# Performance work log

Hardware: AMD Instinct MI355X
Metric: run time of the kernel (lower is better)

Reference implementation:

```python
import jax, jax.numpy as jnp
import numpy as np

N_TABLES = 26
VOCAB = 100000
M_SPA = 64
B = 8192
N_DENSE = 13
N_FEAT = N_TABLES + 1  # 27 features entering interaction
LI, LJ = np.tril_indices(N_FEAT, k=-1)  # strictly-lower pairs, matches torch li/lj order


def setup_inputs() -> dict:
    key = jax.random.key(0)
    ks = jax.random.split(key, 16)
    dense_x = jax.random.normal(ks[0], (B, N_DENSE), dtype=jnp.float32)
    lS_i = jax.random.randint(ks[1], (N_TABLES, B), 0, VOCAB, dtype=jnp.int64)
    # one index per bag -> offsets are arange(B) for every table
    lS_o = jnp.tile(jnp.arange(B, dtype=jnp.int64)[None, :], (N_TABLES, 1))
    # embedding tables, uniform(-sqrt(1/n), sqrt(1/n)) as in create_emb
    s = np.sqrt(1.0 / VOCAB)
    Wemb = jax.random.uniform(ks[2], (N_TABLES, VOCAB, M_SPA), dtype=jnp.float32, minval=-s, maxval=s)

    def mk_lin(k, n, m):
        k1, k2 = jax.random.split(k)
        W = jax.random.normal(k1, (m, n), dtype=jnp.float32) * np.sqrt(2.0 / (m + n))
        b = jax.random.normal(k2, (m,), dtype=jnp.float32) * np.sqrt(1.0 / m)
        return W, b

    bW0, bb0 = mk_lin(ks[3], 13, 512)
    bW1, bb1 = mk_lin(ks[4], 512, 256)
    bW2, bb2 = mk_lin(ks[5], 256, 64)
    tW0, tb0 = mk_lin(ks[6], 415, 512)
    tW1, tb1 = mk_lin(ks[7], 512, 256)
    tW2, tb2 = mk_lin(ks[8], 256, 1)
    return dict(dense_x=dense_x, lS_i=lS_i, lS_o=lS_o, Wemb=Wemb,
                bW0=bW0, bb0=bb0, bW1=bW1, bb1=bb1, bW2=bW2, bb2=bb2,
                tW0=tW0, tb0=tb0, tW1=tW1, tb1=tb1, tW2=tW2, tb2=tb2)


def reference(dense_x, lS_i, lS_o, Wemb,
              bW0, bb0, bW1, bb1, bW2, bb2,
              tW0, tb0, tW1, tb1, tW2, tb2):
    # bottom MLP (all ReLU, sigmoid_bot=-1)
    x = jax.nn.relu(dense_x @ bW0.T + bb0)
    x = jax.nn.relu(x @ bW1.T + bb1)
    x = jax.nn.relu(x @ bW2.T + bb2)  # [B, 64]
    # multi-table EmbeddingBag(sum) with one index per bag == plain gather
    ly = jax.vmap(lambda W, idx: W[idx])(Wemb, lS_i)  # [26, B, 64]
    # dot interaction
    T = jnp.concatenate([x[:, None, :], jnp.transpose(ly, (1, 0, 2))], axis=1)  # [B, 27, 64]
    Z = jnp.einsum('bnd,bmd->bnm', T, T)  # [B, 27, 27]
    Zflat = Z[:, LI, LJ]  # [B, 351]
    R = jnp.concatenate([x, Zflat], axis=1)  # [B, 415]
    # top MLP: ReLU, ReLU, Sigmoid (sigmoid_top=2)
    z = jax.nn.relu(R @ tW0.T + tb0)
    z = jax.nn.relu(z @ tW1.T + tb1)
    p = jax.nn.sigmoid(z @ tW2.T + tb2)  # [B, 1]
    # loss_threshold = 0.0 -> no clamp
    return p
```

## Files before the change

### kernel.cpp

```cpp
#include <hip/hip_runtime.h>
#include <hip/hip_bf16.h>


typedef _Float16 f16x8 __attribute__((ext_vector_type(8)));
typedef float f32x4 __attribute__((ext_vector_type(4)));

__device__ __forceinline__ f16x8 cvt8(float4 a, float4 b) {
  f16x8 f;
  f[0] = (_Float16)a.x; f[1] = (_Float16)a.y;
  f[2] = (_Float16)a.z; f[3] = (_Float16)a.w;
  f[4] = (_Float16)b.x; f[5] = (_Float16)b.y;
  f[6] = (_Float16)b.z; f[7] = (_Float16)b.w;
  return f;
}

__device__ __forceinline__ void tile_store_frag(
    _Float16* __restrict__ dst, const float* __restrict__ src,
    int i, int Ksrc, int NKK)
{
  int e = i & 7;
  int lane = (i >> 3) & 63;
  int rc = lane & 15, g = lane >> 4;
  int q = i >> 9;
  int kk = q % NKK;
  int j = q / NKK;
  int c = j * 16 + rc;
  int k = kk * 32 + g * 8 + e;
  dst[i] = (_Float16)((k < Ksrc) ? src[(size_t)c * Ksrc + k] : 0.0f);
}

__global__ __launch_bounds__(256) void prep_kernel(
    const float* __restrict__ bW0, const float* __restrict__ bW1,
    const float* __restrict__ bW2, const float* __restrict__ tW0,
    const float* __restrict__ tW1,
    _Float16* __restrict__ w0, _Float16* __restrict__ w1,
    _Float16* __restrict__ w2, _Float16* __restrict__ t0,
    _Float16* __restrict__ t1)
{
  int i = blockIdx.x * 256 + threadIdx.x;
  if (i < 16384)  { tile_store_frag(w0, bW0, i, 13, 1);   return; }
  i -= 16384;
  if (i < 131072) { tile_store_frag(w1, bW1, i, 512, 16); return; }
  i -= 131072;
  if (i < 16384)  { tile_store_frag(w2, bW2, i, 256, 8);  return; }
  i -= 16384;
  if (i < 229376) { tile_store_frag(t0, tW0, i, 415, 14); return; }
  i -= 229376;
  if (i < 131072) { tile_store_frag(t1, tW1, i, 512, 16); return; }
}

__global__ __launch_bounds__(512, 2) void fused_kernel(
    const float* __restrict__ dense, const int* __restrict__ lSi,
    const float* __restrict__ Wemb,
    const _Float16* __restrict__ w0, const float* __restrict__ bb0,
    const _Float16* __restrict__ w1, const float* __restrict__ bb1,
    const _Float16* __restrict__ w2, const float* __restrict__ bb2,
    const _Float16* __restrict__ t0w, const float* __restrict__ tb0,
    const _Float16* __restrict__ t1w, const float* __restrict__ tb1,
    const float* __restrict__ tW2, const float* __restrict__ tb2,
    float* __restrict__ out)
{
  __shared__ __align__(16) char regA[32768];
  __shared__ __align__(16) char regB[28672];
  _Float16* x1s = (_Float16*)regA;
  _Float16* x3s = (_Float16*)regA;
  _Float16* z1s = (_Float16*)regA;
  float*    dns = (float*)regB;
  _Float16* x2s = (_Float16*)regB;
  _Float16* Rs  = (_Float16*)regB;
  float*    psm = (float*)regB;

  const int t = threadIdx.x;
  const int lane = t & 63, wv = t >> 6;
  const int rc = lane & 15, g = lane >> 4;
  const int ko = g * 8;
  const int sw = (rc & 7) << 3;
  const int b0 = blockIdx.x * 32;

  if (t < 416) {
    int r = t / 13, c = t - r * 13;
    dns[r * 16 + c] = dense[(size_t)b0 * 13 + t];
  } else if (t < 512) {
    int q = t - 416;
    int r = q / 3, c = 13 + (q - r * 3);
    dns[r * 16 + c] = 0.0f;
  }
  __syncthreads();

  {
    f16x8 af[2];
#pragma unroll
    for (int rt = 0; rt < 2; ++rt) {
      f16x8 a = {};
      if (g < 2) {
        const float* s = &dns[(rt * 16 + rc) * 16 + ko];
        a = cvt8(*(const float4*)s, *(const float4*)(s + 4));
      }
      af[rt] = a;
    }
    f32x4 acc[2][4] = {};
#pragma unroll
    for (int j = 0; j < 4; ++j) {
      const int jb = wv * 4 + j;
      f16x8 wf = *(const f16x8*)&w0[(size_t)(jb * 64 + lane) * 8];
#pragma unroll
      for (int rt = 0; rt < 2; ++rt)
        acc[rt][j] = __builtin_amdgcn_mfma_f32_16x16x32_f16(af[rt], wf, acc[rt][j], 0, 0, 0);
    }
#pragma unroll
    for (int j = 0; j < 4; ++j) {
      const int col = wv * 64 + j * 16 + rc;
      const float bs = bb0[col];
#pragma unroll
      for (int rt = 0; rt < 2; ++rt)
#pragma unroll
        for (int r = 0; r < 4; ++r) {
          int row = rt * 16 + g * 4 + r;
          float v = fmaxf(acc[rt][j][r] + bs, 0.0f);
          x1s[row * 512 + (col ^ ((row & 7) << 3))] = (_Float16)v;
        }
    }
  }
  __syncthreads();

  {
    f32x4 acc[2][2] = {};
#pragma unroll
    for (int kk = 0; kk < 16; ++kk) {
      f16x8 af[2];
#pragma unroll
      for (int rt = 0; rt < 2; ++rt)
        af[rt] = *(const f16x8*)&x1s[(rt * 16 + rc) * 512 + ((kk * 32 + ko) ^ sw)];
#pragma unroll
      for (int j = 0; j < 2; ++j) {
        const int jb = wv * 2 + j;
        f16x8 wf = *(const f16x8*)&w1[(size_t)((jb * 16 + kk) * 64 + lane) * 8];
#pragma unroll
        for (int rt = 0; rt < 2; ++rt)
          acc[rt][j] = __builtin_amdgcn_mfma_f32_16x16x32_f16(af[rt], wf, acc[rt][j], 0, 0, 0);
      }
    }
#pragma unroll
    for (int j = 0; j < 2; ++j) {
      const int col = wv * 32 + j * 16 + rc;
      const float bs = bb1[col];
#pragma unroll
      for (int rt = 0; rt < 2; ++rt)
#pragma unroll
        for (int r = 0; r < 4; ++r) {
          int row = rt * 16 + g * 4 + r;
          float v = fmaxf(acc[rt][j][r] + bs, 0.0f);
          x2s[row * 256 + (col ^ ((row & 7) << 3))] = (_Float16)v;
        }
    }
  }
  __syncthreads();

  if (wv < 4) {
    f32x4 acc[2] = {};
#pragma unroll
    for (int kk = 0; kk < 8; ++kk) {
      f16x8 wf = *(const f16x8*)&w2[(size_t)((wv * 8 + kk) * 64 + lane) * 8];
#pragma unroll
      for (int rt = 0; rt < 2; ++rt) {
        f16x8 af = *(const f16x8*)&x2s[(rt * 16 + rc) * 256 + ((kk * 32 + ko) ^ sw)];
        acc[rt] = __builtin_amdgcn_mfma_f32_16x16x32_f16(af, wf, acc[rt], 0, 0, 0);
      }
    }
    const int col = wv * 16 + rc;
    const float bs = bb2[col];
#pragma unroll
    for (int rt = 0; rt < 2; ++rt)
#pragma unroll
      for (int r = 0; r < 4; ++r) {
        int row = rt * 16 + g * 4 + r;
        float v = fmaxf(acc[rt][r] + bs, 0.0f);
        x3s[row * 64 + col] = (_Float16)v;
      }
  }
  __syncthreads();

  {
    int e_idx[4][2];
#pragma unroll
    for (int i = 0; i < 4; ++i) {
      const int b = b0 + wv * 4 + i;
#pragma unroll
      for (int rt = 0; rt < 2; ++rt) {
        const int gr = rt * 16 + rc;
        e_idx[i][rt] = (gr >= 1 && gr <= 26) ? lSi[(size_t)(gr - 1) * 8192 + b] : 0;
      }
    }
#pragma unroll
    for (int i = 0; i < 4; ++i) {
      const int bl = wv * 4 + i;
      const int swr = (bl & 7) << 3;
      f16x8 frag[2][2];
#pragma unroll
      for (int rt = 0; rt < 2; ++rt) {
        const int gr = rt * 16 + rc;
        if (gr == 0) {
          frag[rt][0] = *(const f16x8*)&x3s[bl * 64 + ko];
          frag[rt][1] = *(const f16x8*)&x3s[bl * 64 + 32 + ko];
        } else if (gr <= 26) {
          const float* src = Wemb + ((size_t)(gr - 1) * 100000 + (size_t)e_idx[i][rt]) * 64;
#pragma unroll
          for (int kh = 0; kh < 2; ++kh) {
            const float* s = src + kh * 32 + ko;
            frag[rt][kh] = cvt8(*(const float4*)s, *(const float4*)(s + 4));
          }
        } else {
          f16x8 z = {};
          frag[rt][0] = z; frag[rt][1] = z;
        }
      }
      f32x4 z00 = {}, z10 = {}, z11 = {};
#pragma unroll
      for (int kh = 0; kh < 2; ++kh) {
        z00 = __builtin_amdgcn_mfma_f32_16x16x32_f16(frag[0][kh], frag[0][kh], z00, 0, 0, 0);
        z10 = __builtin_amdgcn_mfma_f32_16x16x32_f16(frag[1][kh], frag[0][kh], z10, 0, 0, 0);
        z11 = __builtin_amdgcn_mfma_f32_16x16x32_f16(frag[1][kh], frag[1][kh], z11, 0, 0, 0);
      }
      Rs[bl * 448 + (lane ^ swr)] = x3s[bl * 64 + lane];
      if (lane < 33) Rs[bl * 448 + ((415 + lane) ^ swr)] = (_Float16)0.0f;
      const int col = lane & 15;
      const int rr0 = (lane >> 4) * 4;
#pragma unroll
      for (int r = 0; r < 4; ++r) {
        const int i0 = rr0 + r;
        if (i0 > col) {
          int p = 64 + i0 * (i0 - 1) / 2 + col;
          Rs[bl * 448 + (p ^ swr)] = (_Float16)z00[r];
        }
        const int i1 = 16 + rr0 + r;
        if (i1 < 27) {
          int p = 64 + i1 * (i1 - 1) / 2 + col;
          Rs[bl * 448 + (p ^ swr)] = (_Float16)z10[r];
          const int j1 = 16 + col;
          if (i1 > j1) {
            int q = 64 + i1 * (i1 - 1) / 2 + j1;
            Rs[bl * 448 + (q ^ swr)] = (_Float16)z11[r];
          }
        }
      }
    }
  }
  __syncthreads();

  {
    f32x4 acc[2][4] = {};
#pragma unroll
    for (int kk = 0; kk < 14; ++kk) {
      f16x8 af[2];
#pragma unroll
      for (int rt = 0; rt < 2; ++rt)
        af[rt] = *(const f16x8*)&Rs[(rt * 16 + rc) * 448 + ((kk * 32 + ko) ^ sw)];
#pragma unroll
      for (int j = 0; j < 4; ++j) {
        const int jb = wv * 4 + j;
        f16x8 wf = *(const f16x8*)&t0w[(size_t)((jb * 14 + kk) * 64 + lane) * 8];
#pragma unroll
        for (int rt = 0; rt < 2; ++rt)
          acc[rt][j] = __builtin_amdgcn_mfma_f32_16x16x32_f16(af[rt], wf, acc[rt][j], 0, 0, 0);
      }
    }
#pragma unroll
    for (int j = 0; j < 4; ++j) {
      const int col = wv * 64 + j * 16 + rc;
      const float bs = tb0[col];
#pragma unroll
      for (int rt = 0; rt < 2; ++rt)
#pragma unroll
        for (int r = 0; r < 4; ++r) {
          int row = rt * 16 + g * 4 + r;
          float v = fmaxf(acc[rt][j][r] + bs, 0.0f);
          z1s[row * 512 + (col ^ ((row & 7) << 3))] = (_Float16)v;
        }
    }
  }
  __syncthreads();

  {
    f32x4 acc[2][2] = {};
#pragma unroll
    for (int kk = 0; kk < 16; ++kk) {
      f16x8 af[2];
#pragma unroll
      for (int rt = 0; rt < 2; ++rt)
        af[rt] = *(const f16x8*)&z1s[(rt * 16 + rc) * 512 + ((kk * 32 + ko) ^ sw)];
#pragma unroll
      for (int j = 0; j < 2; ++j) {
        const int jb = wv * 2 + j;
        f16x8 wf = *(const f16x8*)&t1w[(size_t)((jb * 16 + kk) * 64 + lane) * 8];
#pragma unroll
        for (int rt = 0; rt < 2; ++rt)
          acc[rt][j] = __builtin_amdgcn_mfma_f32_16x16x32_f16(af[rt], wf, acc[rt][j], 0, 0, 0);
      }
    }
    float pd[2][4];
#pragma unroll
    for (int rt = 0; rt < 2; ++rt)
#pragma unroll
      for (int r = 0; r < 4; ++r) pd[rt][r] = 0.0f;
#pragma unroll
    for (int j = 0; j < 2; ++j) {
      const int col = wv * 32 + j * 16 + rc;
      const float bz = tb1[col];
      const float wz = tW2[col];
#pragma unroll
      for (int rt = 0; rt < 2; ++rt)
#pragma unroll
        for (int r = 0; r < 4; ++r)
          pd[rt][r] += fmaxf(acc[rt][j][r] + bz, 0.0f) * wz;
    }
#pragma unroll
    for (int rt = 0; rt < 2; ++rt)
#pragma unroll
      for (int r = 0; r < 4; ++r) {
        float v = pd[rt][r];
        v += __shfl_xor(v, 1, 64);
        v += __shfl_xor(v, 2, 64);
        v += __shfl_xor(v, 4, 64);
        v += __shfl_xor(v, 8, 64);
        if (rc == 0) psm[wv * 32 + rt * 16 + g * 4 + r] = v;
      }
  }
  __syncthreads();
  if (t < 32) {
    float s = tb2[0];
#pragma unroll
    for (int w = 0; w < 8; ++w) s += psm[w * 32 + t];
    out[b0 + t] = 1.0f / (1.0f + expf(-s));
  }
}

extern "C" void kernel_launch(void* const* d_in, const int* in_sizes, int n_in,
                              void* d_out, int out_size, void* d_ws, size_t ws_size,
                              hipStream_t stream)
{
  (void)in_sizes; (void)n_in; (void)out_size; (void)ws_size;
  const float* dense = (const float*)d_in[0];
  const int*   lSi   = (const int*)d_in[1];
  const float* Wemb  = (const float*)d_in[3];
  const float* bW0 = (const float*)d_in[4];  const float* bb0 = (const float*)d_in[5];
  const float* bW1 = (const float*)d_in[6];  const float* bb1 = (const float*)d_in[7];
  const float* bW2 = (const float*)d_in[8];  const float* bb2 = (const float*)d_in[9];
  const float* tW0 = (const float*)d_in[10]; const float* tb0 = (const float*)d_in[11];
  const float* tW1 = (const float*)d_in[12]; const float* tb1 = (const float*)d_in[13];
  const float* tW2 = (const float*)d_in[14]; const float* tb2 = (const float*)d_in[15];
  float* out = (float*)d_out;

  char* ws = (char*)d_ws;
  size_t off = 0;
  auto alloc = [&](size_t bytes) -> void* {
    void* p = ws + off;
    off += (bytes + 255) & ~(size_t)255;
    return p;
  };
  _Float16* w0 = (_Float16*)alloc((size_t)16384 * 2);
  _Float16* w1 = (_Float16*)alloc((size_t)131072 * 2);
  _Float16* w2 = (_Float16*)alloc((size_t)16384 * 2);
  _Float16* t0 = (_Float16*)alloc((size_t)229376 * 2);
  _Float16* t1 = (_Float16*)alloc((size_t)131072 * 2);

  prep_kernel<<<2048, 256, 0, stream>>>(bW0, bW1, bW2, tW0, tW1,
                                        w0, w1, w2, t0, t1);
  fused_kernel<<<256, 512, 0, stream>>>(dense, lSi, Wemb,
                                        w0, bb0, w1, bb1, w2, bb2,
                                        t0, tb0, t1, tb1, tW2, tb2, out);
}
```

Measured before the change: 39.98 us.

## Halve per-block batch tile to 16 rows and launch 512 blocks

Each block now processes 16 batch rows instead of 32, so the grid doubles to 512 blocks and each wave issues a single 16-row MFMA tile per stage. Shared memory is halved and launch bounds raised to allow more resident blocks, so more of the GPU's compute units get work (256 blocks underfill a large device). In exchange every block re-reads all MLP weights for half as many rows, doubling weight traffic from L2, and MFMA-per-load reuse drops. An extra barrier before the partial-sum reduction protects the reused shared buffer.

Result: slower. 55.35 us (+38.4%).

```diff
diff --git a/kernel.cpp b/kernel.cpp
--- a/kernel.cpp
+++ b/kernel.cpp
@@ -49,7 +49,7 @@
   if (i < 131072) { tile_store_frag(t1, tW1, i, 512, 16); return; }
 }
 
-__global__ __launch_bounds__(512, 2) void fused_kernel(
+__global__ __launch_bounds__(512, 4) void fused_kernel(
     const float* __restrict__ dense, const int* __restrict__ lSi,
     const float* __restrict__ Wemb,
     const _Float16* __restrict__ w0, const float* __restrict__ bb0,
@@ -60,8 +60,8 @@
     const float* __restrict__ tW2, const float* __restrict__ tb2,
     float* __restrict__ out)
 {
-  __shared__ __align__(16) char regA[32768];
-  __shared__ __align__(16) char regB[28672];
+  __shared__ __align__(16) char regA[16384];
+  __shared__ __align__(16) char regB[14336];
   _Float16* x1s = (_Float16*)regA;
   _Float16* x3s = (_Float16*)regA;
   _Float16* z1s = (_Float16*)regA;
@@ -75,69 +75,55 @@
   const int rc = lane & 15, g = lane >> 4;
   const int ko = g * 8;
   const int sw = (rc & 7) << 3;
-  const int b0 = blockIdx.x * 32;
-
-  if (t < 416) {
+  const int b0 = blockIdx.x * 16;
+
+  if (t < 208) {
     int r = t / 13, c = t - r * 13;
     dns[r * 16 + c] = dense[(size_t)b0 * 13 + t];
-  } else if (t < 512) {
-    int q = t - 416;
+  } else if (t < 256) {
+    int q = t - 208;
     int r = q / 3, c = 13 + (q - r * 3);
     dns[r * 16 + c] = 0.0f;
   }
   __syncthreads();
 
   {
-    f16x8 af[2];
-#pragma unroll
-    for (int rt = 0; rt < 2; ++rt) {
-      f16x8 a = {};
-      if (g < 2) {
-        const float* s = &dns[(rt * 16 + rc) * 16 + ko];
-        a = cvt8(*(const float4*)s, *(const float4*)(s + 4));
-      }
-      af[rt] = a;
-    }
-    f32x4 acc[2][4] = {};
+    f16x8 af = {};
+    if (g < 2) {
+      const float* s = &dns[rc * 16 + ko];
+      af = cvt8(*(const float4*)s, *(const float4*)(s + 4));
+    }
+    f32x4 acc[4] = {};
 #pragma unroll
     for (int j = 0; j < 4; ++j) {
       const int jb = wv * 4 + j;
       f16x8 wf = *(const f16x8*)&w0[(size_t)(jb * 64 + lane) * 8];
-#pragma unroll
-      for (int rt = 0; rt < 2; ++rt)
-        acc[rt][j] = __builtin_amdgcn_mfma_f32_16x16x32_f16(af[rt], wf, acc[rt][j], 0, 0, 0);
+      acc[j] = __builtin_amdgcn_mfma_f32_16x16x32_f16(af, wf, acc[j], 0, 0, 0);
     }
 #pragma unroll
     for (int j = 0; j < 4; ++j) {
       const int col = wv * 64 + j * 16 + rc;
       const float bs = bb0[col];
 #pragma unroll
-      for (int rt = 0; rt < 2; ++rt)
-#pragma unroll
-        for (int r = 0; r < 4; ++r) {
-          int row = rt * 16 + g * 4 + r;
-          float v = fmaxf(acc[rt][j][r] + bs, 0.0f);
-          x1s[row * 512 + (col ^ ((row & 7) << 3))] = (_Float16)v;
-        }
-    }
-  }
-  __syncthreads();
-
-  {
-    f32x4 acc[2][2] = {};
+      for (int r = 0; r < 4; ++r) {
+        int row = g * 4 + r;
+        float v = fmaxf(acc[j][r] + bs, 0.0f);
+        x1s[row * 512 + (col ^ ((row & 7) << 3))] = (_Float16)v;
+      }
+    }
+  }
+  __syncthreads();
+
+  {
+    f32x4 acc[2] = {};
 #pragma unroll
     for (int kk = 0; kk < 16; ++kk) {
-      f16x8 af[2];
-#pragma unroll
-      for (int rt = 0; rt < 2; ++rt)
-        af[rt] = *(const f16x8*)&x1s[(rt * 16 + rc) * 512 + ((kk * 32 + ko) ^ sw)];
+      f16x8 af = *(const f16x8*)&x1s[rc * 512 + ((kk * 32 + ko) ^ sw)];
 #pragma unroll
       for (int j = 0; j < 2; ++j) {
         const int jb = wv * 2 + j;
         f16x8 wf = *(const f16x8*)&w1[(size_t)((jb * 16 + kk) * 64 + lane) * 8];
-#pragma unroll
-        for (int rt = 0; rt < 2; ++rt)
-          acc[rt][j] = __builtin_amdgcn_mfma_f32_16x16x32_f16(af[rt], wf, acc[rt][j], 0, 0, 0);
+        acc[j] = __builtin_amdgcn_mfma_f32_16x16x32_f16(af, wf, acc[j], 0, 0, 0);
       }
     }
 #pragma unroll
@@ -145,46 +131,39 @@
       const int col = wv * 32 + j * 16 + rc;
       const float bs = bb1[col];
 #pragma unroll
-      for (int rt = 0; rt < 2; ++rt)
-#pragma unroll
-        for (int r = 0; r < 4; ++r) {
-          int row = rt * 16 + g * 4 + r;
-          float v = fmaxf(acc[rt][j][r] + bs, 0.0f);
-          x2s[row * 256 + (col ^ ((row & 7) << 3))] = (_Float16)v;
-        }
+      for (int r = 0; r < 4; ++r) {
+        int row = g * 4 + r;
+        float v = fmaxf(acc[j][r] + bs, 0.0f);
+        x2s[row * 256 + (col ^ ((row & 7) << 3))] = (_Float16)v;
+      }
     }
   }
   __syncthreads();
 
   if (wv < 4) {
-    f32x4 acc[2] = {};
+    f32x4 acc = {};
 #pragma unroll
     for (int kk = 0; kk < 8; ++kk) {
+      f16x8 af = *(const f16x8*)&x2s[rc * 256 + ((kk * 32 + ko) ^ sw)];
       f16x8 wf = *(const f16x8*)&w2[(size_t)((wv * 8 + kk) * 64 + lane) * 8];
-#pragma unroll
-      for (int rt = 0; rt < 2; ++rt) {
-        f16x8 af = *(const f16x8*)&x2s[(rt * 16 + rc) * 256 + ((kk * 32 + ko) ^ sw)];
-        acc[rt] = __builtin_amdgcn_mfma_f32_16x16x32_f16(af, wf, acc[rt], 0, 0, 0);
-      }
+      acc = __builtin_amdgcn_mfma_f32_16x16x32_f16(af, wf, acc, 0, 0, 0);
     }
     const int col = wv * 16 + rc;
     const float bs = bb2[col];
 #pragma unroll
-    for (int rt = 0; rt < 2; ++rt)
-#pragma unroll
-      for (int r = 0; r < 4; ++r) {
-        int row = rt * 16 + g * 4 + r;
-        float v = fmaxf(acc[rt][r] + bs, 0.0f);
-        x3s[row * 64 + col] = (_Float16)v;
-      }
-  }
-  __syncthreads();
-
-  {
-    int e_idx[4][2];
-#pragma unroll
-    for (int i = 0; i < 4; ++i) {
-      const int b = b0 + wv * 4 + i;
+    for (int r = 0; r < 4; ++r) {
+      int row = g * 4 + r;
+      float v = fmaxf(acc[r] + bs, 0.0f);
+      x3s[row * 64 + col] = (_Float16)v;
+    }
+  }
+  __syncthreads();
+
+  {
+    int e_idx[2][2];
+#pragma unroll
+    for (int i = 0; i < 2; ++i) {
+      const int b = b0 + wv * 2 + i;
 #pragma unroll
       for (int rt = 0; rt < 2; ++rt) {
         const int gr = rt * 16 + rc;
@@ -192,8 +171,8 @@
       }
     }
 #pragma unroll
-    for (int i = 0; i < 4; ++i) {
-      const int bl = wv * 4 + i;
+    for (int i = 0; i < 2; ++i) {
+      const int bl = wv * 2 + i;
       const int swr = (bl & 7) << 3;
       f16x8 frag[2][2];
 #pragma unroll
@@ -248,20 +227,15 @@
   __syncthreads();
 
   {
-    f32x4 acc[2][4] = {};
+    f32x4 acc[4] = {};
 #pragma unroll
     for (int kk = 0; kk < 14; ++kk) {
-      f16x8 af[2];
-#pragma unroll
-      for (int rt = 0; rt < 2; ++rt)
-        af[rt] = *(const f16x8*)&Rs[(rt * 16 + rc) * 448 + ((kk * 32 + ko) ^ sw)];
+      f16x8 af = *(const f16x8*)&Rs[rc * 448 + ((kk * 32 + ko) ^ sw)];
 #pragma unroll
       for (int j = 0; j < 4; ++j) {
         const int jb = wv * 4 + j;
         f16x8 wf = *(const f16x8*)&t0w[(size_t)((jb * 14 + kk) * 64 + lane) * 8];
-#pragma unroll
-        for (int rt = 0; rt < 2; ++rt)
-          acc[rt][j] = __builtin_amdgcn_mfma_f32_16x16x32_f16(af[rt], wf, acc[rt][j], 0, 0, 0);
+        acc[j] = __builtin_amdgcn_mfma_f32_16x16x32_f16(af, wf, acc[j], 0, 0, 0);
       }
     }
 #pragma unroll
@@ -269,67 +243,53 @@
       const int col = wv * 64 + j * 16 + rc;
       const float bs = tb0[col];
 #pragma unroll
-      for (int rt = 0; rt < 2; ++rt)
-#pragma unroll
-        for (int r = 0; r < 4; ++r) {
-          int row = rt * 16 + g * 4 + r;
-          float v = fmaxf(acc[rt][j][r] + bs, 0.0f);
-          z1s[row * 512 + (col ^ ((row & 7) << 3))] = (_Float16)v;
-        }
-    }
-  }
-  __syncthreads();
-
-  {
-    f32x4 acc[2][2] = {};
+      for (int r = 0; r < 4; ++r) {
+        int row = g * 4 + r;
+        float v = fmaxf(acc[j][r] + bs, 0.0f);
+        z1s[row * 512 + (col ^ ((row & 7) << 3))] = (_Float16)v;
+      }
+    }
+  }
+  __syncthreads();
+
+  {
+    f32x4 acc[2] = {};
 #pragma unroll
     for (int kk = 0; kk < 16; ++kk) {
-      f16x8 af[2];
-#pragma unroll
-      for (int rt = 0; rt < 2; ++rt)
-        af[rt] = *(const f16x8*)&z1s[(rt * 16 + rc) * 512 + ((kk * 32 + ko) ^ sw)];
+      f16x8 af = *(const f16x8*)&z1s[rc * 512 + ((kk * 32 + ko) ^ sw)];
 #pragma unroll
       for (int j = 0; j < 2; ++j) {
         const int jb = wv * 2 + j;
         f16x8 wf = *(const f16x8*)&t1w[(size_t)((jb * 16 + kk) * 64 + lane) * 8];
-#pragma unroll
-        for (int rt = 0; rt < 2; ++rt)
-          acc[rt][j] = __builtin_amdgcn_mfma_f32_16x16x32_f16(af[rt], wf, acc[rt][j], 0, 0, 0);
-      }
-    }
-    float pd[2][4];
-#pragma unroll
-    for (int rt = 0; rt < 2; ++rt)
-#pragma unroll
-      for (int r = 0; r < 4; ++r) pd[rt][r] = 0.0f;
+        acc[j] = __builtin_amdgcn_mfma_f32_16x16x32_f16(af, wf, acc[j], 0, 0, 0);
+      }
+    }
+    float pd[4] = {0.0f, 0.0f, 0.0f, 0.0f};
 #pragma unroll
     for (int j = 0; j < 2; ++j) {
       const int col = wv * 32 + j * 16 + rc;
       const float bz = tb1[col];
       const float wz = tW2[col];
 #pragma unroll
-      for (int rt = 0; rt < 2; ++rt)
-#pragma unroll
-        for (int r = 0; r < 4; ++r)
-          pd[rt][r] += fmaxf(acc[rt][j][r] + bz, 0.0f) * wz;
-    }
-#pragma unroll
-    for (int rt = 0; rt < 2; ++rt)
-#pragma unroll
-      for (int r = 0; r < 4; ++r) {
-        float v = pd[rt][r];
-        v += __shfl_xor(v, 1, 64);
-        v += __shfl_xor(v, 2, 64);
-        v += __shfl_xor(v, 4, 64);
-        v += __shfl_xor(v, 8, 64);
-        if (rc == 0) psm[wv * 32 + rt * 16 + g * 4 + r] = v;
-      }
-  }
-  __syncthreads();
-  if (t < 32) {
+      for (int r = 0; r < 4; ++r)
+        pd[r] += fmaxf(acc[j][r] + bz, 0.0f) * wz;
+    }
+    __syncthreads();
+#pragma unroll
+    for (int r = 0; r < 4; ++r) {
+      float v = pd[r];
+      v += __shfl_xor(v, 1, 64);
+      v += __shfl_xor(v, 2, 64);
+      v += __shfl_xor(v, 4, 64);
+      v += __shfl_xor(v, 8, 64);
+      if (rc == 0) psm[wv * 16 + g * 4 + r] = v;
+    }
+  }
+  __syncthreads();
+  if (t < 16) {
     float s = tb2[0];
 #pragma unroll
-    for (int w = 0; w < 8; ++w) s += psm[w * 32 + t];
+    for (int w = 0; w < 8; ++w) s += psm[w * 16 + t];
     out[b0 + t] = 1.0f / (1.0f + expf(-s));
   }
 }
@@ -365,7 +325,7 @@
 
   prep_kernel<<<2048, 256, 0, stream>>>(bW0, bW1, bW2, tW0, tW1,
                                         w0, w1, w2, t0, t1);
-  fused_kernel<<<256, 512, 0, stream>>>(dense, lSi, Wemb,
+  fused_kernel<<<512, 512, 0, stream>>>(dense, lSi, Wemb,
                                         w0, bb0, w1, bb1, w2, bb2,
                                         t0, tb0, t1, tb1, tW2, tb2, out);
 }
```

## Add producer warps that prefetch embedding rows into LDS during bottom MLP

Applied to the files above, without the earlier changes.

Raises the block to 768 threads and dedicates four extra wavefronts to gathering 22 of the 26 embedding tables into swizzled fp16 shared memory while the compute wavefronts run the bottom MLP. The interaction stage then reads those rows from LDS instead of issuing dependent global gathers, and only the last four tables are still fetched directly. The producer waves must match the compute waves' __syncthreads count, which is fragile. The added shared memory (~90KB extra) limits occupancy to one block per CU.

Measured after the change: 49.87 us. 1.25x slower.

```diff
diff --git a/kernel.cpp b/kernel.cpp
--- a/kernel.cpp
+++ b/kernel.cpp
@@ -3,6 +3,7 @@
 
 
 typedef _Float16 f16x8 __attribute__((ext_vector_type(8)));
+typedef _Float16 f16x4 __attribute__((ext_vector_type(4)));
 typedef float f32x4 __attribute__((ext_vector_type(4)));
 
 __device__ __forceinline__ f16x8 cvt8(float4 a, float4 b) {
@@ -49,7 +50,7 @@
   if (i < 131072) { tile_store_frag(t1, tW1, i, 512, 16); return; }
 }
 
-__global__ __launch_bounds__(512, 2) void fused_kernel(
+__global__ __launch_bounds__(768) void fused_kernel(
     const float* __restrict__ dense, const int* __restrict__ lSi,
     const float* __restrict__ Wemb,
     const _Float16* __restrict__ w0, const float* __restrict__ bb0,
@@ -62,6 +63,8 @@
 {
   __shared__ __align__(16) char regA[32768];
   __shared__ __align__(16) char regB[28672];
+  __shared__ __align__(16) _Float16 embs[22 * 32 * 64];
+  __shared__ int idxs[22 * 32];
   _Float16* x1s = (_Float16*)regA;
   _Float16* x3s = (_Float16*)regA;
   _Float16* z1s = (_Float16*)regA;
@@ -77,6 +80,56 @@
   const int sw = (rc & 7) << 3;
   const int b0 = blockIdx.x * 32;
 
+  if (wv >= 8) {
+    const int gw = wv - 8;
+    const int ntab = (gw < 2) ? 6 : 5;
+    const int tbase = (gw < 2) ? gw * 6 : 12 + (gw - 2) * 5;
+#pragma unroll
+    for (int p = 0; p < 3; ++p) {
+      int f = p * 64 + lane;
+      int tl = f >> 5, bl = f & 31;
+      if (tl < ntab)
+        idxs[(tbase + tl) * 32 + bl] = lSi[(size_t)(tbase + tl) * 8192 + b0 + bl];
+    }
+    __syncthreads();
+    const int nq = ntab * 8;
+#pragma unroll
+    for (int c = 0; c < 3; ++c) {
+      float4 v[16];
+#pragma unroll
+      for (int j = 0; j < 16; ++j) {
+        int q = c * 16 + j;
+        int qc = (q < nq) ? q : 0;
+        int fr = qc * 4 + (lane >> 4);
+        int tl = fr >> 5, bl = fr & 31;
+        int idx = idxs[(tbase + tl) * 32 + bl];
+        const float* src =
+            Wemb + ((size_t)(tbase + tl) * 100000 + (size_t)idx) * 64 + (lane & 15) * 4;
+        v[j] = *(const float4*)src;
+      }
+#pragma unroll
+      for (int j = 0; j < 16; ++j) {
+        int q = c * 16 + j;
+        if (q < nq) {
+          int fr = q * 4 + (lane >> 4);
+          int tl = fr >> 5, bl = fr & 31;
+          int tb = tbase + tl;
+          int swe = ((tb + 1) & 7) << 3;
+          int k0 = (lane & 15) * 4;
+          f16x4 h;
+          h[0] = (_Float16)v[j].x; h[1] = (_Float16)v[j].y;
+          h[2] = (_Float16)v[j].z; h[3] = (_Float16)v[j].w;
+          *(f16x4*)&embs[(tb * 32 + bl) * 64 + (k0 ^ swe)] = h;
+        }
+      }
+      __syncthreads();
+    }
+    __syncthreads();
+    __syncthreads();
+    __syncthreads();
+    return;
+  }
+
   if (t < 416) {
     int r = t / 13, c = t - r * 13;
     dns[r * 16 + c] = dense[(size_t)b0 * 13 + t];
@@ -181,16 +234,6 @@
   __syncthreads();
 
   {
-    int e_idx[4][2];
-#pragma unroll
-    for (int i = 0; i < 4; ++i) {
-      const int b = b0 + wv * 4 + i;
-#pragma unroll
-      for (int rt = 0; rt < 2; ++rt) {
-        const int gr = rt * 16 + rc;
-        e_idx[i][rt] = (gr >= 1 && gr <= 26) ? lSi[(size_t)(gr - 1) * 8192 + b] : 0;
-      }
-    }
 #pragma unroll
     for (int i = 0; i < 4; ++i) {
       const int bl = wv * 4 + i;
@@ -202,8 +245,14 @@
         if (gr == 0) {
           frag[rt][0] = *(const f16x8*)&x3s[bl * 64 + ko];
           frag[rt][1] = *(const f16x8*)&x3s[bl * 64 + 32 + ko];
+        } else if (gr <= 22) {
+          const int swe = (gr & 7) << 3;
+          const _Float16* eb = &embs[((gr - 1) * 32 + bl) * 64];
+          frag[rt][0] = *(const f16x8*)&eb[ko ^ swe];
+          frag[rt][1] = *(const f16x8*)&eb[(32 + ko) ^ swe];
         } else if (gr <= 26) {
-          const float* src = Wemb + ((size_t)(gr - 1) * 100000 + (size_t)e_idx[i][rt]) * 64;
+          int idx = lSi[(size_t)(gr - 1) * 8192 + b0 + bl];
+          const float* src = Wemb + ((size_t)(gr - 1) * 100000 + (size_t)idx) * 64;
 #pragma unroll
           for (int kh = 0; kh < 2; ++kh) {
             const float* s = src + kh * 32 + ko;
@@ -365,7 +414,7 @@
 
   prep_kernel<<<2048, 256, 0, stream>>>(bW0, bW1, bW2, tW0, tW1,
                                         w0, w1, w2, t0, t1);
-  fused_kernel<<<256, 512, 0, stream>>>(dense, lSi, Wemb,
+  fused_kernel<<<256, 768, 0, stream>>>(dense, lSi, Wemb,
                                         w0, bb0, w1, bb1, w2, bb2,
                                         t0, tb0, t1, tb1, tW2, tb2, out);
 }
```

## Use 1024-thread blocks, splitting each layer's columns across 16 waves

Applied to the files above, without the earlier changes.

Doubles the block size from 512 to 1024 threads (16 waves) and halves the per-wave output-column share in every MLP layer, the embedding gather and the interaction stage. The grid stays at 256 blocks, so each CU gets more waves in flight to hide the latency of the global weight and embedding loads. In exchange, launch bounds fall to one block per CU with a tighter register budget, and a barrier plus a 16-way partial-sum reduction are added. The psm shared buffer must now hold 16 partial-sum slots per row instead of 8.

Result: faster. 36.84 us (-7.8%).

```diff
diff --git a/kernel.cpp b/kernel.cpp
--- a/kernel.cpp
+++ b/kernel.cpp
@@ -49,7 +49,7 @@
   if (i < 131072) { tile_store_frag(t1, tW1, i, 512, 16); return; }
 }
 
-__global__ __launch_bounds__(512, 2) void fused_kernel(
+__global__ __launch_bounds__(1024, 1) void fused_kernel(
     const float* __restrict__ dense, const int* __restrict__ lSi,
     const float* __restrict__ Wemb,
     const _Float16* __restrict__ w0, const float* __restrict__ bb0,
@@ -98,18 +98,18 @@
       }
       af[rt] = a;
     }
-    f32x4 acc[2][4] = {};
-#pragma unroll
-    for (int j = 0; j < 4; ++j) {
-      const int jb = wv * 4 + j;
+    f32x4 acc[2][2] = {};
+#pragma unroll
+    for (int j = 0; j < 2; ++j) {
+      const int jb = wv * 2 + j;
       f16x8 wf = *(const f16x8*)&w0[(size_t)(jb * 64 + lane) * 8];
 #pragma unroll
       for (int rt = 0; rt < 2; ++rt)
         acc[rt][j] = __builtin_amdgcn_mfma_f32_16x16x32_f16(af[rt], wf, acc[rt][j], 0, 0, 0);
     }
 #pragma unroll
-    for (int j = 0; j < 4; ++j) {
-      const int col = wv * 64 + j * 16 + rc;
+    for (int j = 0; j < 2; ++j) {
+      const int col = wv * 32 + j * 16 + rc;
       const float bs = bb0[col];
 #pragma unroll
       for (int rt = 0; rt < 2; ++rt)
@@ -124,67 +124,57 @@
   __syncthreads();
 
   {
-    f32x4 acc[2][2] = {};
+    f32x4 acc[2] = {};
 #pragma unroll
     for (int kk = 0; kk < 16; ++kk) {
       f16x8 af[2];
 #pragma unroll
       for (int rt = 0; rt < 2; ++rt)
         af[rt] = *(const f16x8*)&x1s[(rt * 16 + rc) * 512 + ((kk * 32 + ko) ^ sw)];
-#pragma unroll
-      for (int j = 0; j < 2; ++j) {
-        const int jb = wv * 2 + j;
-        f16x8 wf = *(const f16x8*)&w1[(size_t)((jb * 16 + kk) * 64 + lane) * 8];
-#pragma unroll
-        for (int rt = 0; rt < 2; ++rt)
-          acc[rt][j] = __builtin_amdgcn_mfma_f32_16x16x32_f16(af[rt], wf, acc[rt][j], 0, 0, 0);
-      }
-    }
-#pragma unroll
-    for (int j = 0; j < 2; ++j) {
-      const int col = wv * 32 + j * 16 + rc;
-      const float bs = bb1[col];
-#pragma unroll
-      for (int rt = 0; rt < 2; ++rt)
-#pragma unroll
-        for (int r = 0; r < 4; ++r) {
-          int row = rt * 16 + g * 4 + r;
-          float v = fmaxf(acc[rt][j][r] + bs, 0.0f);
-          x2s[row * 256 + (col ^ ((row & 7) << 3))] = (_Float16)v;
-        }
-    }
-  }
-  __syncthreads();
-
-  if (wv < 4) {
-    f32x4 acc[2] = {};
-#pragma unroll
-    for (int kk = 0; kk < 8; ++kk) {
-      f16x8 wf = *(const f16x8*)&w2[(size_t)((wv * 8 + kk) * 64 + lane) * 8];
-#pragma unroll
-      for (int rt = 0; rt < 2; ++rt) {
-        f16x8 af = *(const f16x8*)&x2s[(rt * 16 + rc) * 256 + ((kk * 32 + ko) ^ sw)];
-        acc[rt] = __builtin_amdgcn_mfma_f32_16x16x32_f16(af, wf, acc[rt], 0, 0, 0);
-      }
+      f16x8 wf = *(const f16x8*)&w1[(size_t)((wv * 16 + kk) * 64 + lane) * 8];
+#pragma unroll
+      for (int rt = 0; rt < 2; ++rt)
+        acc[rt] = __builtin_amdgcn_mfma_f32_16x16x32_f16(af[rt], wf, acc[rt], 0, 0, 0);
     }
     const int col = wv * 16 + rc;
-    const float bs = bb2[col];
+    const float bs = bb1[col];
 #pragma unroll
     for (int rt = 0; rt < 2; ++rt)
 #pragma unroll
       for (int r = 0; r < 4; ++r) {
         int row = rt * 16 + g * 4 + r;
         float v = fmaxf(acc[rt][r] + bs, 0.0f);
-        x3s[row * 64 + col] = (_Float16)v;
-      }
-  }
-  __syncthreads();
-
-  {
-    int e_idx[4][2];
-#pragma unroll
-    for (int i = 0; i < 4; ++i) {
-      const int b = b0 + wv * 4 + i;
+        x2s[row * 256 + (col ^ ((row & 7) << 3))] = (_Float16)v;
+      }
+  }
+  __syncthreads();
+
+  if (wv < 8) {
+    const int rt = wv & 1;
+    const int cb = (wv >> 1) * 16;
+    f32x4 acc = {};
+#pragma unroll
+    for (int kk = 0; kk < 8; ++kk) {
+      f16x8 af = *(const f16x8*)&x2s[(rt * 16 + rc) * 256 + ((kk * 32 + ko) ^ sw)];
+      f16x8 wf = *(const f16x8*)&w2[(size_t)(((cb >> 4) * 8 + kk) * 64 + lane) * 8];
+      acc = __builtin_amdgcn_mfma_f32_16x16x32_f16(af, wf, acc, 0, 0, 0);
+    }
+    const int col = cb + rc;
+    const float bs = bb2[col];
+#pragma unroll
+    for (int r = 0; r < 4; ++r) {
+      int row = rt * 16 + g * 4 + r;
+      float v = fmaxf(acc[r] + bs, 0.0f);
+      x3s[row * 64 + col] = (_Float16)v;
+    }
+  }
+  __syncthreads();
+
+  {
+    int e_idx[2][2];
+#pragma unroll
+    for (int i = 0; i < 2; ++i) {
+      const int b = b0 + wv * 2 + i;
 #pragma unroll
       for (int rt = 0; rt < 2; ++rt) {
         const int gr = rt * 16 + rc;
@@ -192,8 +182,8 @@
       }
     }
 #pragma unroll
-    for (int i = 0; i < 4; ++i) {
-      const int bl = wv * 4 + i;
+    for (int i = 0; i < 2; ++i) {
+      const int bl = wv * 2 + i;
       const int swr = (bl & 7) << 3;
       f16x8 frag[2][2];
 #pragma unroll
@@ -248,7 +238,7 @@
   __syncthreads();
 
   {
-    f32x4 acc[2][4] = {};
+    f32x4 acc[2][2] = {};
 #pragma unroll
     for (int kk = 0; kk < 14; ++kk) {
       f16x8 af[2];
@@ -256,8 +246,8 @@
       for (int rt = 0; rt < 2; ++rt)
         af[rt] = *(const f16x8*)&Rs[(rt * 16 + rc) * 448 + ((kk * 32 + ko) ^ sw)];
 #pragma unroll
-      for (int j = 0; j < 4; ++j) {
-        const int jb = wv * 4 + j;
+      for (int j = 0; j < 2; ++j) {
+        const int jb = wv * 2 + j;
         f16x8 wf = *(const f16x8*)&t0w[(size_t)((jb * 14 + kk) * 64 + lane) * 8];
 #pragma unroll
         for (int rt = 0; rt < 2; ++rt)
@@ -265,8 +255,8 @@
       }
     }
 #pragma unroll
-    for (int j = 0; j < 4; ++j) {
-      const int col = wv * 64 + j * 16 + rc;
+    for (int j = 0; j < 2; ++j) {
+      const int col = wv * 32 + j * 16 + rc;
       const float bs = tb0[col];
 #pragma unroll
       for (int rt = 0; rt < 2; ++rt)
@@ -281,38 +271,28 @@
   __syncthreads();
 
   {
-    f32x4 acc[2][2] = {};
+    f32x4 acc[2] = {};
 #pragma unroll
     for (int kk = 0; kk < 16; ++kk) {
       f16x8 af[2];
 #pragma unroll
       for (int rt = 0; rt < 2; ++rt)
         af[rt] = *(const f16x8*)&z1s[(rt * 16 + rc) * 512 + ((kk * 32 + ko) ^ sw)];
-#pragma unroll
-      for (int j = 0; j < 2; ++j) {
-        const int jb = wv * 2 + j;
-        f16x8 wf = *(const f16x8*)&t1w[(size_t)((jb * 16 + kk) * 64 + lane) * 8];
-#pragma unroll
-        for (int rt = 0; rt < 2; ++rt)
-          acc[rt][j] = __builtin_amdgcn_mfma_f32_16x16x32_f16(af[rt], wf, acc[rt][j], 0, 0, 0);
-      }
-    }
+      f16x8 wf = *(const f16x8*)&t1w[(size_t)((wv * 16 + kk) * 64 + lane) * 8];
+#pragma unroll
+      for (int rt = 0; rt < 2; ++rt)
+        acc[rt] = __builtin_amdgcn_mfma_f32_16x16x32_f16(af[rt], wf, acc[rt], 0, 0, 0);
+    }
+    const int col = wv * 16 + rc;
+    const float bz = tb1[col];
+    const float wz = tW2[col];
     float pd[2][4];
 #pragma unroll
     for (int rt = 0; rt < 2; ++rt)
 #pragma unroll
-      for (int r = 0; r < 4; ++r) pd[rt][r] = 0.0f;
-#pragma unroll
-    for (int j = 0; j < 2; ++j) {
-      const int col = wv * 32 + j * 16 + rc;
-      const float bz = tb1[col];
-      const float wz = tW2[col];
-#pragma unroll
-      for (int rt = 0; rt < 2; ++rt)
-#pragma unroll
-        for (int r = 0; r < 4; ++r)
-          pd[rt][r] += fmaxf(acc[rt][j][r] + bz, 0.0f) * wz;
-    }
+      for (int r = 0; r < 4; ++r)
+        pd[rt][r] = fmaxf(acc[rt][r] + bz, 0.0f) * wz;
+    __syncthreads();
 #pragma unroll
     for (int rt = 0; rt < 2; ++rt)
 #pragma unroll
@@ -329,7 +309,7 @@
   if (t < 32) {
     float s = tb2[0];
 #pragma unroll
-    for (int w = 0; w < 8; ++w) s += psm[w * 32 + t];
+    for (int w = 0; w < 16; ++w) s += psm[w * 32 + t];
     out[b0 + t] = 1.0f / (1.0f + expf(-s));
   }
 }
@@ -365,7 +345,7 @@
 
   prep_kernel<<<2048, 256, 0, stream>>>(bW0, bW1, bW2, tW0, tW1,
                                         w0, w1, w2, t0, t1);
-  fused_kernel<<<256, 512, 0, stream>>>(dense, lSi, Wemb,
-                                        w0, bb0, w1, bb1, w2, bb2,
-                                        t0, tb0, t1, tb1, tW2, tb2, out);
-}
+  fused_kernel<<<256, 1024, 0, stream>>>(dense, lSi, Wemb,
+                                         w0, bb0, w1, bb1, w2, bb2,
+                                         t0, tb0, t1, tb1, tW2, tb2, out);
+}
```
